# Optimization experiments

Measured on AMD Instinct MI355X. Metric: run time of the kernel, lower is better.

## Reference

```python
import jax, jax.numpy as jnp
import numpy as np

SIGMA = 1.0
RADIUS = 4        # int(truncate * sigma + 0.5), skimage default truncate=4.0
NBINS = 256       # skimage threshold_otsu default
MEAN, STD = 0.5, 0.5


def _gauss_kernel():
    xs = np.arange(-RADIUS, RADIUS + 1, dtype=np.float32)
    k = np.exp(-0.5 * (xs / SIGMA) ** 2)
    return jnp.asarray(k / k.sum())


def _blur(img):
    # img: [B, H, W]; skimage gaussian(sigma=1) == separable conv, 'nearest' (edge) padding
    k = _gauss_kernel()
    p = jnp.pad(img, ((0, 0), (RADIUS, RADIUS), (RADIUS, RADIUS)), mode='edge')
    x = p[:, None]  # [B,1,H+2R,W+2R]
    x = jax.lax.conv_general_dilated(x, k.reshape(1, 1, -1, 1), (1, 1), 'VALID')
    x = jax.lax.conv_general_dilated(x, k.reshape(1, 1, 1, -1), (1, 1), 'VALID')
    return x[:, 0]


def _otsu(img):
    # Otsu threshold over a 256-bin histogram spanning [min, max] (skimage semantics)
    mn, mx = img.min(), img.max()
    rng = jnp.maximum(mx - mn, 1e-12)
    idx = jnp.clip(jnp.floor((img - mn) / rng * NBINS).astype(jnp.int32), 0, NBINS - 1)
    hist = jnp.zeros(NBINS, jnp.float32).at[idx.ravel()].add(1.0)
    centers = mn + (jnp.arange(NBINS, dtype=jnp.float32) + 0.5) * (rng / NBINS)
    w1 = jnp.cumsum(hist)
    w2 = jnp.cumsum(hist[::-1])[::-1]
    m1 = jnp.cumsum(hist * centers) / jnp.maximum(w1, 1e-12)
    m2 = jnp.cumsum((hist * centers)[::-1])[::-1] / jnp.maximum(w2, 1e-12)
    var12 = w1[:-1] * w2[1:] * (m1[:-1] - m2[1:]) ** 2
    return centers[jnp.argmax(var12)]


def setup_inputs() -> dict:
    key = jax.random.key(0)
    x = jax.random.normal(key, (32, 4, 512, 512), dtype=jnp.float32)
    return {"x": x}


def reference(x):
    # thershold_mask on thermal channel: denormalize (mul std, add mean), clamp, blur, Otsu
    thermal = jnp.clip(x[:, 0] * STD + MEAN, 0.0, 1.0)          # [B,H,W]
    blurred = _blur(thermal)                                     # [B,H,W]
    t = jax.vmap(_otsu)(blurred)                                 # [B]
    mask = jnp.where(blurred > t[:, None, None], 1.0, blurred)   # soft mask
    # rgba2rgb with white background: out = alpha*rgb + (1-alpha)*1, clipped to [0,1]
    rgb = x[:, -3:]                                              # [B,3,H,W]
    alpha = mask[:, None]                                        # [B,1,H,W]
    out_rgb = jnp.clip(alpha * rgb + (1.0 - alpha), 0.0, 1.0)
    # use_thermal=True: replace last 3 channels, keep thermal channel
    return x.at[:, 1:4].set(out_rgb)
```

## Files before the change

kernel.cpp:

```cpp
#include <hip/hip_runtime.h>
#include <math.h>

#define NIMG 32
#define HWDIM 512
#define NPIX (HWDIM * HWDIM)
#define NB 256
#define RAD 4
#define TW 64
#define TH 64

struct W9 { float w[9]; };

__device__ __forceinline__ float clip01(float v) { return fminf(fmaxf(v, 0.0f), 1.0f); }

static float np_expf(float x) {
  const float LOG2E = 1.442695040f;
  const float CW_HI = -6.93145752e-1f;
  const float CW_LO = -1.42860677e-6f;
  const float P0 = 9.999999999980870924916e-01f;
  const float P1 = 7.257664613233124478488e-01f;
  const float P2 = 2.473615434895520810817e-01f;
  const float P3 = 5.114512081637298353406e-02f;
  const float P4 = 6.757896990527504603057e-03f;
  const float P5 = 5.082762527590693718096e-04f;
  const float Q0 = 1.000000000000000000000e+00f;
  const float Q1 = -2.742335390411667452936e-01f;
  const float Q2 = 2.159509375685829852307e-02f;
  float m = rintf(x * LOG2E);
  float y = fmaf(m, CW_HI, x);
  y = fmaf(m, CW_LO, y);
  float num = fmaf(fmaf(fmaf(fmaf(fmaf(P5, y, P4), y, P3), y, P2), y, P1), y, P0);
  float den = fmaf(fmaf(Q2, y, Q1), y, Q0);
  float r = num / den;
  return ldexpf(r, (int)m);
}

__global__ __launch_bounds__(256) void blur_kernel(const float* __restrict__ x, float* __restrict__ out,
                                                   float* __restrict__ mnmx, W9 wp) {
  __shared__ float raw[TH + 8][TW + 8];
  __shared__ float vb[TH][TW + 8];
  const int img = blockIdx.z;
  const int blk = blockIdx.y * 8 + blockIdx.x;
  const int tx0 = blockIdx.x * TW;
  const int ty0 = blockIdx.y * TH;
  const float* src = x + (size_t)img * 4 * NPIX;
  float* out0 = out + (size_t)img * 4 * NPIX;
  float* bl = out0 + NPIX;
  const int tid = threadIdx.x;

  for (int i = tid; i < (TH + 8) * (TW + 8); i += 256) {
    int lr = i / (TW + 8), lc = i % (TW + 8);
    int gr = ty0 - RAD + lr; gr = gr < 0 ? 0 : (gr > HWDIM - 1 ? HWDIM - 1 : gr);
    int gc = tx0 - RAD + lc; gc = gc < 0 ? 0 : (gc > HWDIM - 1 ? HWDIM - 1 : gc);
    float v = src[gr * HWDIM + gc];
    if (lr >= RAD && lr < RAD + TH && lc >= RAD && lc < RAD + TW)
      out0[gr * HWDIM + gc] = v;
    raw[lr][lc] = clip01(__fadd_rn(__fmul_rn(v, 0.5f), 0.5f));
  }
  __syncthreads();

  for (int i = tid; i < TH * (TW + 8); i += 256) {
    int r = i / (TW + 8), c = i % (TW + 8);
    double acc = 0.0;
#pragma unroll
    for (int k = 0; k < 9; ++k) acc += (double)wp.w[k] * (double)raw[r + k][c];
    vb[r][c] = (float)acc;
  }
  __syncthreads();

  float lmn = __int_as_float(0x7F800000);
  float lmx = 0.0f;
  for (int i = tid; i < TH * TW; i += 256) {
    int r = i >> 6, c = i & 63;
    double acc = 0.0;
#pragma unroll
    for (int k = 0; k < 9; ++k) acc += (double)wp.w[k] * (double)vb[r][c + k];
    float a = (float)acc;
    bl[(ty0 + r) * HWDIM + (tx0 + c)] = a;
    lmn = fminf(lmn, a);
    lmx = fmaxf(lmx, a);
  }
  for (int off = 32; off > 0; off >>= 1) {
    lmn = fminf(lmn, __shfl_down(lmn, off, 64));
    lmx = fmaxf(lmx, __shfl_down(lmx, off, 64));
  }
  __shared__ float smn[4], smx[4];
  if ((tid & 63) == 0) { smn[tid >> 6] = lmn; smx[tid >> 6] = lmx; }
  __syncthreads();
  if (tid == 0) {
    float mnb = fminf(fminf(smn[0], smn[1]), fminf(smn[2], smn[3]));
    float mxb = fmaxf(fmaxf(smx[0], smx[1]), fmaxf(smx[2], smx[3]));
    mnmx[img * 128 + blk * 2] = mnb;
    mnmx[img * 128 + blk * 2 + 1] = mxb;
  }
}

__global__ __launch_bounds__(256) void hist_kernel(const float* __restrict__ mnmx, float* __restrict__ out) {
  __shared__ int lh[4 * 260];
  __shared__ float s_mn, s_mx;
  const int img = blockIdx.y;
  const int p = blockIdx.x;
  const int tid = threadIdx.x;
  for (int i = tid; i < 4 * 260; i += 256) lh[i] = 0;

  float lmn = __int_as_float(0x7F800000);
  float lmx = 0.0f;
  if (tid < 64) {
    lmn = mnmx[img * 128 + tid * 2];
    lmx = mnmx[img * 128 + tid * 2 + 1];
  }
  if (tid < 64) {
    for (int off = 32; off > 0; off >>= 1) {
      lmn = fminf(lmn, __shfl_down(lmn, off, 64));
      lmx = fmaxf(lmx, __shfl_down(lmx, off, 64));
    }
    if (tid == 0) { s_mn = lmn; s_mx = lmx; }
  }
  __syncthreads();
  const float mn = s_mn;
  const float mx = s_mx;
  const float rng = fmaxf(mx - mn, 1e-12f);

  const float4* src = (const float4*)(out + (size_t)img * 4 * NPIX + NPIX);
  int* my = lh + (tid & 3) * 260;
#pragma unroll
  for (int j = 0; j < 4; ++j) {
    float4 v = src[p * 1024 + j * 256 + tid];
    float q; int b;
    q = __fmul_rn(__fdiv_rn(__fsub_rn(v.x, mn), rng), 256.0f); b = (int)floorf(q); b = b < 0 ? 0 : (b > 255 ? 255 : b); atomicAdd(&my[b], 1);
    q = __fmul_rn(__fdiv_rn(__fsub_rn(v.y, mn), rng), 256.0f); b = (int)floorf(q); b = b < 0 ? 0 : (b > 255 ? 255 : b); atomicAdd(&my[b], 1);
    q = __fmul_rn(__fdiv_rn(__fsub_rn(v.z, mn), rng), 256.0f); b = (int)floorf(q); b = b < 0 ? 0 : (b > 255 ? 255 : b); atomicAdd(&my[b], 1);
    q = __fmul_rn(__fdiv_rn(__fsub_rn(v.w, mn), rng), 256.0f); b = (int)floorf(q); b = b < 0 ? 0 : (b > 255 ? 255 : b); atomicAdd(&my[b], 1);
  }
  __syncthreads();
  int c = lh[tid] + lh[260 + tid] + lh[2 * 260 + tid] + lh[3 * 260 + tid];
  int* part = (int*)(out + (size_t)img * 4 * NPIX + 2 * NPIX);
  part[p * NB + tid] = c;
}

__global__ __launch_bounds__(256) void otsu_kernel(const float* __restrict__ mnmx, const float* __restrict__ out,
                                                   float* __restrict__ t) {
  __shared__ int h[NB];
  __shared__ float rs[NB + 1];
  __shared__ float s_mn, s_mx;
  const int img = blockIdx.x;
  const int tid = threadIdx.x;
  const int* part = (const int*)(out + (size_t)img * 4 * NPIX + 2 * NPIX);
  int sum = 0;
#pragma unroll 8
  for (int p = 0; p < 64; ++p) sum += part[p * NB + tid];
  h[tid] = sum;

  float lmn = __int_as_float(0x7F800000);
  float lmx = 0.0f;
  if (tid < 64) {
    lmn = mnmx[img * 128 + tid * 2];
    lmx = mnmx[img * 128 + tid * 2 + 1];
    for (int off = 32; off > 0; off >>= 1) {
      lmn = fminf(lmn, __shfl_down(lmn, off, 64));
      lmx = fmaxf(lmx, __shfl_down(lmx, off, 64));
    }
    if (tid == 0) { s_mn = lmn; s_mx = lmx; }
  }
  __syncthreads();
  if (tid != 0) return;

  const float mn = s_mn;
  const float mx = s_mx;
  const float rng = fmaxf(mx - mn, 1e-12f);
  const float scale = rng / 256.0f;

  float acc = 0.0f;
  rs[NB] = 0.0f;
  for (int i = NB - 1; i >= 0; --i) {
    float c = __fadd_rn(mn, __fmul_rn((float)i + 0.5f, scale));
    acc = __fadd_rn(acc, __fmul_rn((float)h[i], c));
    rs[i] = acc;
  }

  float w1 = 0.0f, cs1 = 0.0f, best = -INFINITY;
  int arg = 0;
  for (int i = 0; i < NB - 1; ++i) {
    float hi = (float)h[i];
    float c = __fadd_rn(mn, __fmul_rn((float)i + 0.5f, scale));
    w1 = __fadd_rn(w1, hi);
    cs1 = __fadd_rn(cs1, __fmul_rn(hi, c));
    float w2n = (float)NPIX - w1;
    float m1 = __fdiv_rn(cs1, fmaxf(w1, 1e-12f));
    float m2n = __fdiv_rn(rs[i + 1], fmaxf(w2n, 1e-12f));
    float d = __fsub_rn(m1, m2n);
    float v = __fmul_rn(__fmul_rn(w1, w2n), __fmul_rn(d, d));
    if (v > best) { best = v; arg = i; }
  }
  t[img] = __fadd_rn(mn, __fmul_rn((float)arg + 0.5f, scale));
}

__global__ __launch_bounds__(256) void mask_kernel(const float* __restrict__ x, const float* __restrict__ tarr,
                                                   float* __restrict__ out) {
  const int gid = blockIdx.x * 256 + threadIdx.x;
  const int img = gid >> 16;
  const int rem = gid & 65535;
  const float4* xb = (const float4*)(x + (size_t)img * 4 * NPIX);
  float4* ob = (float4*)(out + (size_t)img * 4 * NPIX);
  const float tv = tarr[img];

  float4 bl = ob[65536 + rem];
  float4 x1 = xb[65536 + rem];
  float4 x2 = xb[2 * 65536 + rem];
  float4 x3 = xb[3 * 65536 + rem];

  float a0 = bl.x > tv ? 1.0f : bl.x;
  float a1 = bl.y > tv ? 1.0f : bl.y;
  float a2 = bl.z > tv ? 1.0f : bl.z;
  float a3 = bl.w > tv ? 1.0f : bl.w;

  float4 o1, o2, o3;
  o1.x = clip01(__fadd_rn(__fmul_rn(a0, x1.x), 1.0f - a0));
  o1.y = clip01(__fadd_rn(__fmul_rn(a1, x1.y), 1.0f - a1));
  o1.z = clip01(__fadd_rn(__fmul_rn(a2, x1.z), 1.0f - a2));
  o1.w = clip01(__fadd_rn(__fmul_rn(a3, x1.w), 1.0f - a3));
  o2.x = clip01(__fadd_rn(__fmul_rn(a0, x2.x), 1.0f - a0));
  o2.y = clip01(__fadd_rn(__fmul_rn(a1, x2.y), 1.0f - a1));
  o2.z = clip01(__fadd_rn(__fmul_rn(a2, x2.z), 1.0f - a2));
  o2.w = clip01(__fadd_rn(__fmul_rn(a3, x2.w), 1.0f - a3));
  o3.x = clip01(__fadd_rn(__fmul_rn(a0, x3.x), 1.0f - a0));
  o3.y = clip01(__fadd_rn(__fmul_rn(a1, x3.y), 1.0f - a1));
  o3.z = clip01(__fadd_rn(__fmul_rn(a2, x3.z), 1.0f - a2));
  o3.w = clip01(__fadd_rn(__fmul_rn(a3, x3.w), 1.0f - a3));

  ob[65536 + rem] = o1;
  ob[2 * 65536 + rem] = o2;
  ob[3 * 65536 + rem] = o3;
}

extern "C" void kernel_launch(void* const* d_in, const int* in_sizes, int n_in,
                              void* d_out, int out_size, void* d_ws, size_t ws_size,
                              hipStream_t stream) {
  const float* x = (const float*)d_in[0];
  float* out = (float*)d_out;
  char* ws = (char*)d_ws;
  float* mnmx = (float*)(ws + 0);
  float* t = (float*)(ws + 32 * 128 * 4);

  W9 wp;
  {
    float k[9];
    for (int i = 0; i < 9; ++i) {
      float xs = (float)(i - 4);
      float argv = -0.5f * (xs * xs);
      k[i] = np_expf(argv);
    }
    float s = ((k[0] + k[1]) + (k[2] + k[3])) + ((k[4] + k[5]) + (k[6] + k[7]));
    s = s + k[8];
    for (int i = 0; i < 9; ++i) wp.w[i] = k[i] / s;
  }

  hipLaunchKernelGGL(blur_kernel, dim3(HWDIM / TW, HWDIM / TH, NIMG), dim3(256), 0, stream,
                     x, out, mnmx, wp);
  hipLaunchKernelGGL(hist_kernel, dim3(64, NIMG), dim3(256), 0, stream, mnmx, out);
  hipLaunchKernelGGL(otsu_kernel, dim3(NIMG), dim3(256), 0, stream, mnmx, out, t);
  hipLaunchKernelGGL(mask_kernel, dim3(NIMG * NPIX / 4 / 256), dim3(256), 0, stream,
                     x, t, out);
}
```

Baseline: 134.6 us.

## Fuse histogram and Otsu kernels into one per-image block; vectorize blur stores

Merges the histogram and Otsu kernels into a single 1024-thread block per image. This removes the partial-histogram round trip through global memory and one kernel launch. The blur kernel now writes the channel-0 passthrough copy and the blurred output as coalesced float4 stores, and each thread computes four horizontal outputs. The catch is that the histogram stage now runs on only 32 blocks, one per image, so each block streams 1 MB. That cuts parallelism sharply on a GPU with many CUs and may make the histogram phase slower.

```diff
diff --git a/kernel.cpp b/kernel.cpp
--- a/kernel.cpp
+++ b/kernel.cpp
@@ -53,9 +53,18 @@
     int gr = ty0 - RAD + lr; gr = gr < 0 ? 0 : (gr > HWDIM - 1 ? HWDIM - 1 : gr);
     int gc = tx0 - RAD + lc; gc = gc < 0 ? 0 : (gc > HWDIM - 1 ? HWDIM - 1 : gc);
     float v = src[gr * HWDIM + gc];
-    if (lr >= RAD && lr < RAD + TH && lc >= RAD && lc < RAD + TW)
-      out0[gr * HWDIM + gc] = v;
     raw[lr][lc] = clip01(__fadd_rn(__fmul_rn(v, 0.5f), 0.5f));
+  }
+  {
+    const float4* s4 = (const float4*)src;
+    float4* o4 = (float4*)out0;
+#pragma unroll
+    for (int it = 0; it < 4; ++it) {
+      int g = tid + it * 256;
+      int r = g >> 4, c4 = g & 15;
+      int idx = (ty0 + r) * (HWDIM / 4) + (tx0 >> 2) + c4;
+      o4[idx] = s4[idx];
+    }
   }
   __syncthreads();
 
@@ -70,15 +79,25 @@
 
   float lmn = __int_as_float(0x7F800000);
   float lmx = 0.0f;
-  for (int i = tid; i < TH * TW; i += 256) {
-    int r = i >> 6, c = i & 63;
-    double acc = 0.0;
-#pragma unroll
-    for (int k = 0; k < 9; ++k) acc += (double)wp.w[k] * (double)vb[r][c + k];
-    float a = (float)acc;
-    bl[(ty0 + r) * HWDIM + (tx0 + c)] = a;
-    lmn = fminf(lmn, a);
-    lmx = fmaxf(lmx, a);
+  float4* bl4 = (float4*)bl;
+#pragma unroll
+  for (int it = 0; it < 4; ++it) {
+    int g = tid + it * 256;
+    int r = g >> 4, c0 = (g & 15) * 4;
+    double a0 = 0.0, a1 = 0.0, a2 = 0.0, a3 = 0.0;
+#pragma unroll
+    for (int k = 0; k < 9; ++k) {
+      double wk = (double)wp.w[k];
+      a0 += wk * (double)vb[r][c0 + k];
+      a1 += wk * (double)vb[r][c0 + 1 + k];
+      a2 += wk * (double)vb[r][c0 + 2 + k];
+      a3 += wk * (double)vb[r][c0 + 3 + k];
+    }
+    float4 o;
+    o.x = (float)a0; o.y = (float)a1; o.z = (float)a2; o.w = (float)a3;
+    bl4[(ty0 + r) * (HWDIM / 4) + (tx0 >> 2) + (g & 15)] = o;
+    lmn = fminf(lmn, fminf(fminf(o.x, o.y), fminf(o.z, o.w)));
+    lmx = fmaxf(lmx, fmaxf(fmaxf(o.x, o.y), fmaxf(o.z, o.w)));
   }
   for (int off = 32; off > 0; off >>= 1) {
     lmn = fminf(lmn, __shfl_down(lmn, off, 64));
@@ -95,21 +114,20 @@
   }
 }
 
-__global__ __launch_bounds__(256) void hist_kernel(const float* __restrict__ mnmx, float* __restrict__ out) {
-  __shared__ int lh[4 * 260];
+__global__ __launch_bounds__(1024) void histotsu_kernel(const float* __restrict__ mnmx,
+                                                        const float* __restrict__ out,
+                                                        float* __restrict__ t) {
+  __shared__ int lh[8 * 260];
+  __shared__ int h[NB];
+  __shared__ float rs[NB + 1];
   __shared__ float s_mn, s_mx;
-  const int img = blockIdx.y;
-  const int p = blockIdx.x;
+  const int img = blockIdx.x;
   const int tid = threadIdx.x;
-  for (int i = tid; i < 4 * 260; i += 256) lh[i] = 0;
-
-  float lmn = __int_as_float(0x7F800000);
-  float lmx = 0.0f;
+  for (int i = tid; i < 8 * 260; i += 1024) lh[i] = 0;
+
   if (tid < 64) {
-    lmn = mnmx[img * 128 + tid * 2];
-    lmx = mnmx[img * 128 + tid * 2 + 1];
-  }
-  if (tid < 64) {
+    float lmn = mnmx[img * 128 + tid * 2];
+    float lmx = mnmx[img * 128 + tid * 2 + 1];
     for (int off = 32; off > 0; off >>= 1) {
       lmn = fminf(lmn, __shfl_down(lmn, off, 64));
       lmx = fmaxf(lmx, __shfl_down(lmx, off, 64));
@@ -118,14 +136,13 @@
   }
   __syncthreads();
   const float mn = s_mn;
-  const float mx = s_mx;
-  const float rng = fmaxf(mx - mn, 1e-12f);
+  const float rng = fmaxf(s_mx - mn, 1e-12f);
 
   const float4* src = (const float4*)(out + (size_t)img * 4 * NPIX + NPIX);
-  int* my = lh + (tid & 3) * 260;
-#pragma unroll
-  for (int j = 0; j < 4; ++j) {
-    float4 v = src[p * 1024 + j * 256 + tid];
+  int* my = lh + (tid & 7) * 260;
+#pragma unroll 4
+  for (int j = 0; j < 64; ++j) {
+    float4 v = src[j * 1024 + tid];
     float q; int b;
     q = __fmul_rn(__fdiv_rn(__fsub_rn(v.x, mn), rng), 256.0f); b = (int)floorf(q); b = b < 0 ? 0 : (b > 255 ? 255 : b); atomicAdd(&my[b], 1);
     q = __fmul_rn(__fdiv_rn(__fsub_rn(v.y, mn), rng), 256.0f); b = (int)floorf(q); b = b < 0 ? 0 : (b > 255 ? 255 : b); atomicAdd(&my[b], 1);
@@ -133,43 +150,16 @@
     q = __fmul_rn(__fdiv_rn(__fsub_rn(v.w, mn), rng), 256.0f); b = (int)floorf(q); b = b < 0 ? 0 : (b > 255 ? 255 : b); atomicAdd(&my[b], 1);
   }
   __syncthreads();
-  int c = lh[tid] + lh[260 + tid] + lh[2 * 260 + tid] + lh[3 * 260 + tid];
-  int* part = (int*)(out + (size_t)img * 4 * NPIX + 2 * NPIX);
-  part[p * NB + tid] = c;
-}
-
-__global__ __launch_bounds__(256) void otsu_kernel(const float* __restrict__ mnmx, const float* __restrict__ out,
-                                                   float* __restrict__ t) {
-  __shared__ int h[NB];
-  __shared__ float rs[NB + 1];
-  __shared__ float s_mn, s_mx;
-  const int img = blockIdx.x;
-  const int tid = threadIdx.x;
-  const int* part = (const int*)(out + (size_t)img * 4 * NPIX + 2 * NPIX);
-  int sum = 0;
-#pragma unroll 8
-  for (int p = 0; p < 64; ++p) sum += part[p * NB + tid];
-  h[tid] = sum;
-
-  float lmn = __int_as_float(0x7F800000);
-  float lmx = 0.0f;
-  if (tid < 64) {
-    lmn = mnmx[img * 128 + tid * 2];
-    lmx = mnmx[img * 128 + tid * 2 + 1];
-    for (int off = 32; off > 0; off >>= 1) {
-      lmn = fminf(lmn, __shfl_down(lmn, off, 64));
-      lmx = fmaxf(lmx, __shfl_down(lmx, off, 64));
-    }
-    if (tid == 0) { s_mn = lmn; s_mx = lmx; }
+  if (tid < NB) {
+    int c = 0;
+#pragma unroll
+    for (int s = 0; s < 8; ++s) c += lh[s * 260 + tid];
+    h[tid] = c;
   }
   __syncthreads();
   if (tid != 0) return;
 
-  const float mn = s_mn;
-  const float mx = s_mx;
-  const float rng = fmaxf(mx - mn, 1e-12f);
   const float scale = rng / 256.0f;
-
   float acc = 0.0f;
   rs[NB] = 0.0f;
   for (int i = NB - 1; i >= 0; --i) {
@@ -177,7 +167,6 @@
     acc = __fadd_rn(acc, __fmul_rn((float)h[i], c));
     rs[i] = acc;
   }
-
   float w1 = 0.0f, cs1 = 0.0f, best = -INFINITY;
   int arg = 0;
   for (int i = 0; i < NB - 1; ++i) {
@@ -257,8 +246,7 @@
 
   hipLaunchKernelGGL(blur_kernel, dim3(HWDIM / TW, HWDIM / TH, NIMG), dim3(256), 0, stream,
                      x, out, mnmx, wp);
-  hipLaunchKernelGGL(hist_kernel, dim3(64, NIMG), dim3(256), 0, stream, mnmx, out);
-  hipLaunchKernelGGL(otsu_kernel, dim3(NIMG), dim3(256), 0, stream, mnmx, out, t);
+  hipLaunchKernelGGL(histotsu_kernel, dim3(NIMG), dim3(1024), 0, stream, mnmx, out, t);
   hipLaunchKernelGGL(mask_kernel, dim3(NIMG * NPIX / 4 / 256), dim3(256), 0, stream,
                      x, t, out);
 }
```

Result: slower. 151.3 us (+12.4%).
